# Kernel tuning notes

Hardware: AMD Instinct MI355X
Metric: run time of the kernel (lower is better)

## Reference

```python
import jax, jax.numpy as jnp
import numpy as np

GAP = 1.0
THRESHOLD = 0.1


def setup_inputs() -> dict:
    key = jax.random.key(0)
    k1, k2 = jax.random.split(key)
    B = 8192
    return {
        "input": jax.random.normal(k1, (B, 1), dtype=jnp.float32),
        "gdt_ts": jax.random.uniform(k2, (B,), dtype=jnp.float32),
    }


def reference(input, gdt_ts):
    # o: [B] predicted scores
    o = jnp.squeeze(input)
    B = o.shape[0]
    # pairwise label differences [B, B]
    ld = gdt_ts[:, None] - gdt_ts[None, :]
    # y_ij = -1 if tm_i < tm_j else +1 (ties -> +1, matching torch code)
    y = jnp.where(ld < 0, -1.0, 1.0).astype(o.dtype)
    # example weight: 1 if |tm_i - tm_j| > threshold else 0
    # (diagonal has ld == 0 so weight 0 -> i == j pairs drop out automatically)
    w = (jnp.abs(ld) > THRESHOLD).astype(o.dtype)
    # hinge: max(0, gap + y_ij * (o_i - o_j))
    hinge = jnp.maximum(0.0, GAP + y * (o[:, None] - o[None, :]))
    N = B * (B - 1)  # number of ordered i != j pairs
    loss = jnp.sum(w * hinge) / N
    return loss[None]  # shape [1], matching the torch module
```

## Files before the change

kernel.cpp:

```cpp
#include <hip/hip_runtime.h>


constexpr int BLOCK  = 256;
constexpr int TILE_I = 4;
constexpr int JCHUNK = 64;
constexpr float GAP = 1.0f;
constexpr float THRESHOLD = 0.1f;

__global__ __launch_bounds__(BLOCK) void pair_loss_kernel(
        const float* __restrict__ o, const float* __restrict__ t,
        float* __restrict__ partials) {
    __shared__ float so[JCHUNK];
    __shared__ float st[JCHUNK];

    const int tid = threadIdx.x;
    const int j0  = blockIdx.y * JCHUNK;

    if (tid < JCHUNK)                 so[tid] = o[j0 + tid];
    else if (tid < 2 * JCHUNK)        st[tid - JCHUNK] = t[j0 + tid - JCHUNK];
    __syncthreads();

    const int ibase = blockIdx.x * (BLOCK * TILE_I) + tid;
    float oi[TILE_I], ti[TILE_I];
#pragma unroll
    for (int k = 0; k < TILE_I; ++k) {
        oi[k] = o[ibase + k * BLOCK];
        ti[k] = t[ibase + k * BLOCK];
    }

    float acc[TILE_I] = {0.f, 0.f, 0.f, 0.f};
#pragma unroll 8
    for (int j = 0; j < JCHUNK; ++j) {
        const float oj = so[j];
        const float tj = st[j];
#pragma unroll
        for (int k = 0; k < TILE_I; ++k) {
            const float ld   = ti[k] - tj;
            const float diff = oi[k] - oj;
            const unsigned sgn = __float_as_uint(ld) & 0x80000000u;
            const float yd  = __uint_as_float(__float_as_uint(diff) ^ sgn);
            const float s   = GAP + yd;
            acc[k] += (fabsf(ld) > THRESHOLD) ? fmaxf(s, 0.0f) : 0.0f;
        }
    }

    float a = (acc[0] + acc[1]) + (acc[2] + acc[3]);
    for (int off = 32; off > 0; off >>= 1)
        a += __shfl_down(a, off, 64);

    __shared__ float wsum[BLOCK / 64];
    if ((tid & 63) == 0) wsum[tid >> 6] = a;
    __syncthreads();

    if (tid == 0) {
        float s = 0.0f;
#pragma unroll
        for (int w = 0; w < BLOCK / 64; ++w) s += wsum[w];
        partials[blockIdx.y * gridDim.x + blockIdx.x] = s;
    }
}

__global__ __launch_bounds__(BLOCK) void reduce_kernel(
        const float* __restrict__ partials, float* __restrict__ out,
        int nblk, int B) {
    const int tid = threadIdx.x;
    float a = 0.0f;
    for (int p = tid; p < nblk; p += BLOCK) a += partials[p];

    for (int off = 32; off > 0; off >>= 1)
        a += __shfl_down(a, off, 64);

    __shared__ float wsum[BLOCK / 64];
    if ((tid & 63) == 0) wsum[tid >> 6] = a;
    __syncthreads();

    if (tid == 0) {
        float s = 0.0f;
#pragma unroll
        for (int w = 0; w < BLOCK / 64; ++w) s += wsum[w];
        const float N = (float)((long long)B * (long long)(B - 1));
        out[0] = s / N;
    }
}

extern "C" void kernel_launch(void* const* d_in, const int* in_sizes, int n_in,
                              void* d_out, int out_size, void* d_ws, size_t ws_size,
                              hipStream_t stream) {
    const float* o = (const float*)d_in[0];
    const float* t = (const float*)d_in[1];
    float* out = (float*)d_out;
    float* ws  = (float*)d_ws;

    const int B = in_sizes[1];

    dim3 grid(B / (BLOCK * TILE_I), B / JCHUNK);
    pair_loss_kernel<<<grid, BLOCK, 0, stream>>>(o, t, ws);

    const int nblk = grid.x * grid.y;
    reduce_kernel<<<1, BLOCK, 0, stream>>>(ws, out, nblk, B);
}
```

Baseline: 69.89 us.

## Exploit pair symmetry to compute only lower-triangular tiles and double the sum

After: 72.23 us. 1.03x slower.

```diff
diff --git a/kernel.cpp b/kernel.cpp
--- a/kernel.cpp
+++ b/kernel.cpp
@@ -3,46 +3,69 @@
 
 constexpr int BLOCK  = 256;
 constexpr int TILE_I = 4;
+constexpr int ITILE  = BLOCK * TILE_I;
 constexpr int JCHUNK = 64;
 constexpr float GAP = 1.0f;
 constexpr float THRESHOLD = 0.1f;
 
-__global__ __launch_bounds__(BLOCK) void pair_loss_kernel(
-        const float* __restrict__ o, const float* __restrict__ t,
-        float* __restrict__ partials) {
-    __shared__ float so[JCHUNK];
-    __shared__ float st[JCHUNK];
-
-    const int tid = threadIdx.x;
-    const int j0  = blockIdx.y * JCHUNK;
-
-    if (tid < JCHUNK)                 so[tid] = o[j0 + tid];
-    else if (tid < 2 * JCHUNK)        st[tid - JCHUNK] = t[j0 + tid - JCHUNK];
-    __syncthreads();
-
-    const int ibase = blockIdx.x * (BLOCK * TILE_I) + tid;
-    float oi[TILE_I], ti[TILE_I];
-#pragma unroll
-    for (int k = 0; k < TILE_I; ++k) {
-        oi[k] = o[ibase + k * BLOCK];
-        ti[k] = t[ibase + k * BLOCK];
-    }
-
-    float acc[TILE_I] = {0.f, 0.f, 0.f, 0.f};
+template <bool MASK>
+__device__ __forceinline__ void pair_tile(
+        const float* so, const float* st,
+        const float* oi, const float* ti,
+        const int* ig, int j0, float* acc) {
 #pragma unroll 8
     for (int j = 0; j < JCHUNK; ++j) {
         const float oj = so[j];
         const float tj = st[j];
+        const int  jg = j0 + j;
 #pragma unroll
         for (int k = 0; k < TILE_I; ++k) {
             const float ld   = ti[k] - tj;
             const float diff = oi[k] - oj;
             const unsigned sgn = __float_as_uint(ld) & 0x80000000u;
-            const float yd  = __uint_as_float(__float_as_uint(diff) ^ sgn);
-            const float s   = GAP + yd;
-            acc[k] += (fabsf(ld) > THRESHOLD) ? fmaxf(s, 0.0f) : 0.0f;
+            const float yd = __uint_as_float(__float_as_uint(diff) ^ sgn);
+            const float h  = fmaxf(GAP + yd, 0.0f);
+            bool cond = fabsf(ld) > THRESHOLD;
+            if (MASK) cond = cond && (jg < ig[k]);
+            acc[k] += cond ? h : 0.0f;
         }
     }
+}
+
+__global__ __launch_bounds__(BLOCK) void pair_loss_kernel(
+        const float* __restrict__ o, const float* __restrict__ t,
+        float* __restrict__ partials) {
+    const int tid = threadIdx.x;
+    const int i0  = blockIdx.x * ITILE;
+    const int j0  = blockIdx.y * JCHUNK;
+    const int pidx = blockIdx.y * gridDim.x + blockIdx.x;
+
+    if (j0 >= i0 + ITILE) {
+        if (tid == 0) partials[pidx] = 0.0f;
+        return;
+    }
+
+    __shared__ float so[JCHUNK];
+    __shared__ float st[JCHUNK];
+    if (tid < JCHUNK)          so[tid] = o[j0 + tid];
+    else if (tid < 2 * JCHUNK) st[tid - JCHUNK] = t[j0 + tid - JCHUNK];
+    __syncthreads();
+
+    const int ibase = i0 + tid;
+    float oi[TILE_I], ti[TILE_I];
+    int   ig[TILE_I];
+#pragma unroll
+    for (int k = 0; k < TILE_I; ++k) {
+        ig[k] = ibase + k * BLOCK;
+        oi[k] = o[ig[k]];
+        ti[k] = t[ig[k]];
+    }
+
+    float acc[TILE_I] = {0.f, 0.f, 0.f, 0.f};
+    if (j0 + JCHUNK <= i0)
+        pair_tile<false>(so, st, oi, ti, ig, j0, acc);
+    else
+        pair_tile<true>(so, st, oi, ti, ig, j0, acc);
 
     float a = (acc[0] + acc[1]) + (acc[2] + acc[3]);
     for (int off = 32; off > 0; off >>= 1)
@@ -56,7 +79,7 @@
         float s = 0.0f;
 #pragma unroll
         for (int w = 0; w < BLOCK / 64; ++w) s += wsum[w];
-        partials[blockIdx.y * gridDim.x + blockIdx.x] = s;
+        partials[pidx] = s;
     }
 }
 
@@ -79,7 +102,7 @@
 #pragma unroll
         for (int w = 0; w < BLOCK / 64; ++w) s += wsum[w];
         const float N = (float)((long long)B * (long long)(B - 1));
-        out[0] = s / N;
+        out[0] = 2.0f * s / N;
     }
 }
 
@@ -93,7 +116,7 @@
 
     const int B = in_sizes[1];
 
-    dim3 grid(B / (BLOCK * TILE_I), B / JCHUNK);
+    dim3 grid(B / ITILE, B / JCHUNK);
     pair_loss_kernel<<<grid, BLOCK, 0, stream>>>(o, t, ws);
 
     const int nblk = grid.x * grid.y;
```
